# Performance work log

Hardware: AMD Instinct MI355X
Metric: run time of the kernel (lower is better)

Reference implementation:

```python
import jax, jax.numpy as jnp
import numpy as np

RENDER_STEP = 0.005
N_FREQS = 6

def pos_enc(x):
    # x: [N,3] -> [N, 3 + 2*N_FREQS*3]
    freqs = (2.0 ** jnp.arange(N_FREQS, dtype=x.dtype)) * jnp.pi
    xb = x[:, None, :] * freqs[:, None]            # [N,F,3]
    enc = jnp.concatenate([jnp.sin(xb), jnp.cos(xb)], axis=-1).reshape(x.shape[0], -1)
    return jnp.concatenate([x, enc], axis=-1)

def geom_fwd(points, Wg0, bg0, Wg1, bg1, Wg2, bg2):
    h = jax.nn.relu(pos_enc(points) @ Wg0 + bg0)
    h = jax.nn.relu(h @ Wg1 + bg1)
    return h @ Wg2 + bg2                           # [N,16]; ch0 = sdf, full vec = features


def setup_inputs() -> dict:
    key = jax.random.key(0)
    ks = jax.random.split(key, 12)
    n_rays, n_samples = 16384, 524288
    sc = lambda fan_in: 1.0 / np.sqrt(fan_in)
    inp = {
        'rays_o': jax.random.normal(ks[0], (n_rays, 3), jnp.float32) * 0.5,
        'rays_d': jax.random.normal(ks[1], (n_rays, 3), jnp.float32),
        'ray_indices': jnp.sort(jax.random.randint(ks[2], (n_samples,), 0, n_rays, jnp.int32)),
        't_starts': jax.random.uniform(ks[3], (n_samples, 1), jnp.float32),
        'random_points': jax.random.normal(ks[4], (1024, 3), jnp.float32),
        's_var': jnp.ones((1,), jnp.float32),
        'Wg0': jax.random.normal(ks[5], (39, 256), jnp.float32) * sc(39),
        'bg0': jnp.zeros((256,), jnp.float32),
        'Wg1': jax.random.normal(ks[6], (256, 256), jnp.float32) * sc(256),
        'bg1': jnp.zeros((256,), jnp.float32),
        'Wg2': jax.random.normal(ks[7], (256, 16), jnp.float32) * sc(256),
        'bg2': jnp.zeros((16,), jnp.float32),
        'Wc0': jax.random.normal(ks[8], (25, 256), jnp.float32) * sc(25),
        'bc0': jnp.zeros((256,), jnp.float32),
        'Wc1': jax.random.normal(ks[9], (256, 3), jnp.float32) * sc(256),
        'bc1': jnp.zeros((3,), jnp.float32),
    }
    return inp


def reference(rays_o, rays_d, ray_indices, t_starts, random_points, s_var,
              Wg0, bg0, Wg1, bg1, Wg2, bg2, Wc0, bc0, Wc1, bc1):
    n_rays = rays_o.shape[0]
    rays_d = rays_d / (jnp.linalg.norm(rays_d, axis=-1, keepdims=True) + 1e-10)

    midpoints = t_starts + RENDER_STEP * 0.5       # [N,1]
    t_intervals = RENDER_STEP
    t_origins = rays_o[ray_indices]                # gather [N,3]
    t_dirs = rays_d[ray_indices]
    points = t_origins + t_dirs * midpoints        # [N,3]

    # SDF network forward + analytic gradient wrt points (one fwd + one bwd)
    out, vjp_fn = jax.vjp(lambda p: geom_fwd(p, Wg0, bg0, Wg1, bg1, Wg2, bg2), points)
    sdf = out[:, 0]                                # [N]
    feats = out                                    # [N,16]
    cot = jnp.zeros_like(out).at[:, 0].set(1.0)
    grad = vjp_fn(cot)[0]                          # dSDF/dpoints [N,3]
    normal = grad / (jnp.linalg.norm(grad, axis=-1, keepdims=True) + 1e-10)

    # color network: dirs + feats + points + normal -> rgb
    cin = jnp.concatenate([t_dirs, feats, points, normal], axis=-1)   # [N,25]
    rgbs = jax.nn.sigmoid(jax.nn.relu(cin @ Wc0 + bc0) @ Wc1 + bc1)   # [N,3]

    # get_alpha (cos_anneal_ratio = 1.0)
    inv_s = jnp.clip(jnp.exp(s_var[0]), 1e-6, 1e6)
    dSDF_dt = jnp.sum(grad * t_dirs, axis=-1, keepdims=True)
    dSDF_dt = -jax.nn.relu(-dSDF_dt)
    cdf = jax.nn.sigmoid(inv_s * sdf[:, None])
    rho = jnp.maximum(inv_s * (cdf - 1.0) * dSDF_dt, 0.0)
    alpha = 1.0 - jnp.exp(-rho * t_intervals)      # [N,1]

    # render_weight_from_alpha: per-ray exclusive cumprod of (1-alpha), log-space
    a = jnp.clip(alpha[:, 0], 0.0, 1.0 - 1e-7)
    loga = jnp.log1p(-a)
    E = jnp.cumsum(loga) - loga                    # exclusive cumsum
    starts = jnp.clip(jnp.searchsorted(ray_indices, jnp.arange(n_rays, dtype=ray_indices.dtype)),
                      0, a.shape[0] - 1)           # first sample idx per ray
    trans = jnp.exp(E - E[starts][ray_indices])    # per-ray transmittance
    weights = (a * trans)[:, None]                 # [N,1]

    seg = lambda v: jax.ops.segment_sum(weights * v, ray_indices, num_segments=n_rays)
    opacity = jax.ops.segment_sum(weights, ray_indices, num_segments=n_rays)  # [R,1]
    depth = seg(midpoints)
    pixels_color = seg(rgbs)
    pixels_normal = seg(normal)
    pixels_normal = pixels_normal / (jnp.linalg.norm(pixels_normal, axis=-1, keepdims=True) + 1e-10)

    random_sdfs = geom_fwd(random_points, Wg0, bg0, Wg1, bg1, Wg2, bg2)[:, :1]
    return (pixels_color, pixels_normal, opacity, depth, weights, sdf, random_sdfs)
```

## Files before the change

kernel.cpp:

```cpp
#include <hip/hip_runtime.h>
#include <math.h>


#define TILE 32
#define NTHREADS 512
#define LDP 264
#define LDE 72
#define LDCIN 40
#define PI_F 3.14159265358979323846f

typedef _Float16 half8 __attribute__((ext_vector_type(8)));
typedef float f32x4 __attribute__((ext_vector_type(4)));
typedef float f32x16 __attribute__((ext_vector_type(16)));

struct alignas(16) SMemK2 {
    _Float16 a0h[TILE * LDP];
    _Float16 a0l[TILE * LDP];
    _Float16 a1h[TILE * LDP];
    _Float16 a1l[TILE * LDP];
    _Float16 ench[TILE * LDE];
    _Float16 encl[TILE * LDE];
    float feats[TILE * 16];
    float pts [TILE * 4];
    float dirs[TILE * 4];
    float nrm [TILE * 4];
};

__device__ __forceinline__ void splitst(float v, _Float16* ph, _Float16* pl) {
    _Float16 h = (_Float16)v;
    *ph = h;
    *pl = (_Float16)(v - (float)h);
}

__device__ __forceinline__ f32x16 zero16() {
    f32x16 z;
#pragma unroll
    for (int i = 0; i < 16; ++i) z[i] = 0.f;
    return z;
}

template<int KITERS, bool BIAS, bool RELU, bool AMASK, bool CMASK>
__device__ __forceinline__ void gemm32(
    const _Float16* Ah, const _Float16* Al, const int lda,
    const _Float16* __restrict__ Bp, const float* __restrict__ bias,
    _Float16* Ch, _Float16* Cl, const int ldc,
    const int lane, const int nt)
{
    f32x16 acc0 = zero16(), acc1 = zero16();
    const int row  = lane & 31;
    const int koff = (lane >> 5) * 8;
    const _Float16* ahb = Ah + row * lda + koff;
    const _Float16* alb = Al + row * lda + koff;
    const _Float16* bbase = Bp + ((size_t)nt * KITERS * 64 + lane) * 16;

    half8 bh[2], bl[2], ax[2], ay[2];
    bh[0] = *(const half8*)bbase;
    bl[0] = *(const half8*)(bbase + 8);
    ax[0] = *(const half8*)ahb;
    if (!AMASK) ay[0] = *(const half8*)alb;

#pragma unroll
    for (int kit = 0; kit < KITERS; ++kit) {
        const int cur = kit & 1, nxt = cur ^ 1;
        if (kit + 1 < KITERS) {
            const _Float16* bp = bbase + (size_t)(kit + 1) * 1024;
            bh[nxt] = *(const half8*)bp;
            bl[nxt] = *(const half8*)(bp + 8);
            ax[nxt] = *(const half8*)(ahb + (kit + 1) * 16);
            if (!AMASK) ay[nxt] = *(const half8*)(alb + (kit + 1) * 16);
        }
        f32x16& acc = (kit & 1) ? acc1 : acc0;
        if (AMASK) {
            half8 m;
#pragma unroll
            for (int j = 0; j < 8; ++j) {
                _Float16 t = ax[cur][j] * (_Float16)16384.f;
                m[j] = (t < (_Float16)1.f) ? t : (_Float16)1.f;
            }
            __builtin_amdgcn_s_setprio(1);
            acc = __builtin_amdgcn_mfma_f32_32x32x16_f16(m, bh[cur], acc, 0, 0, 0);
            acc = __builtin_amdgcn_mfma_f32_32x32x16_f16(m, bl[cur], acc, 0, 0, 0);
            __builtin_amdgcn_s_setprio(0);
        } else {
            __builtin_amdgcn_s_setprio(1);
            acc = __builtin_amdgcn_mfma_f32_32x32x16_f16(ay[cur], bh[cur], acc, 0, 0, 0);
            acc = __builtin_amdgcn_mfma_f32_32x32x16_f16(ax[cur], bl[cur], acc, 0, 0, 0);
            acc = __builtin_amdgcn_mfma_f32_32x32x16_f16(ax[cur], bh[cur], acc, 0, 0, 0);
            __builtin_amdgcn_s_setprio(0);
        }
    }
    const int col = lane & 31;
    const int rb  = (lane >> 5) * 4;
    const int jc  = nt * 32 + col;
    const float bs = BIAS ? bias[jc] : 0.f;
#pragma unroll
    for (int r = 0; r < 16; ++r) {
        const int srow = (r & 3) + 8 * (r >> 2) + rb;
        float v = acc0[r] + acc1[r] + bs;
        if (RELU) v = (v > 0.f) ? fmaxf(v, 1e-4f) : 0.f;
        if (CMASK) { if (!((float)Ch[srow * ldc + jc] > 0.f)) v = 0.f; }
        _Float16 h = (_Float16)v;
        Ch[srow * ldc + jc] = h;
        Cl[srow * ldc + jc] = (_Float16)(v - (float)h);
    }
}

template<int KITERS, int NTPW>
__device__ __forceinline__ void gemm16(
    const _Float16* Ah, const _Float16* Al, const int lda,
    const _Float16* __restrict__ Bp,
    _Float16* Ch, _Float16* Cl, const int ldc,
    const int lane, const int mt, const int ntbase)
{
    f32x4 acc[NTPW];
#pragma unroll
    for (int t = 0; t < NTPW; ++t) acc[t] = (f32x4){0.f, 0.f, 0.f, 0.f};
    const int m  = mt * 16 + (lane & 15);
    const int q8 = (lane >> 4) * 8;
    const _Float16* ahb = Ah + m * lda + q8;
    const _Float16* alb = Al + m * lda + q8;
    const _Float16* bbase = Bp + ((size_t)ntbase * KITERS * 64 + lane) * 16;

    half8 ax[2], ay[2], bh[2][NTPW], bl[2][NTPW];
    ax[0] = *(const half8*)ahb;
    ay[0] = *(const half8*)alb;
#pragma unroll
    for (int t = 0; t < NTPW; ++t) {
        const _Float16* bt = bbase + (size_t)t * KITERS * 1024;
        bh[0][t] = *(const half8*)bt;
        bl[0][t] = *(const half8*)(bt + 8);
    }
#pragma unroll
    for (int kit = 0; kit < KITERS; ++kit) {
        const int cur = kit & 1, nxt = cur ^ 1;
        if (kit + 1 < KITERS) {
            ax[nxt] = *(const half8*)(ahb + (kit + 1) * 32);
            ay[nxt] = *(const half8*)(alb + (kit + 1) * 32);
            const _Float16* bp = bbase + (size_t)(kit + 1) * 1024;
#pragma unroll
            for (int t = 0; t < NTPW; ++t) {
                const _Float16* bt = bp + (size_t)t * KITERS * 1024;
                bh[nxt][t] = *(const half8*)bt;
                bl[nxt][t] = *(const half8*)(bt + 8);
            }
        }
        __builtin_amdgcn_s_setprio(1);
#pragma unroll
        for (int t = 0; t < NTPW; ++t) {
            acc[t] = __builtin_amdgcn_mfma_f32_16x16x32_f16(ay[cur], bh[cur][t], acc[t], 0, 0, 0);
            acc[t] = __builtin_amdgcn_mfma_f32_16x16x32_f16(ax[cur], bl[cur][t], acc[t], 0, 0, 0);
            acc[t] = __builtin_amdgcn_mfma_f32_16x16x32_f16(ax[cur], bh[cur][t], acc[t], 0, 0, 0);
        }
        __builtin_amdgcn_s_setprio(0);
    }
    const int col = lane & 15, q = lane >> 4;
#pragma unroll
    for (int t = 0; t < NTPW; ++t) {
        const int j = (ntbase + t) * 16 + col;
#pragma unroll
        for (int r = 0; r < 4; ++r) {
            const int s = mt * 16 + q * 4 + r;
            float v = acc[t][r];
            _Float16 h = (_Float16)v;
            Ch[s * ldc + j] = h;
            Cl[s * ldc + j] = (_Float16)(v - (float)h);
        }
    }
}

__global__ __launch_bounds__(256) void k0_pack(
    const float* __restrict__ Wg0, const float* __restrict__ Wg1,
    const float* __restrict__ Wg2, const float* __restrict__ Wc0,
    const float* __restrict__ Wc1,
    _Float16* __restrict__ Wg0p, _Float16* __restrict__ Wg1p,
    _Float16* __restrict__ Wg1Tp, _Float16* __restrict__ Wg0Tp,
    _Float16* __restrict__ Wc0p, _Float16* __restrict__ Wg2p,
    _Float16* __restrict__ Wc1p)
{
    int gid = blockIdx.x * 256 + threadIdx.x;
    if (gid >= 180224) return;
    int idx, kiters, mode;
    _Float16* dst;
    if      (gid <  16384) { idx = gid;          kiters = 4;  dst = Wg0p;  mode = 0; }
    else if (gid <  81920) { idx = gid -  16384; kiters = 16; dst = Wg1p;  mode = 1; }
    else if (gid < 147456) { idx = gid -  81920; kiters = 16; dst = Wg1Tp; mode = 2; }
    else if (gid < 163840) { idx = gid - 147456; kiters = 8;  dst = Wg0Tp; mode = 3; }
    else if (gid < 172032) { idx = gid - 163840; kiters = 2;  dst = Wc0p;  mode = 4; }
    else if (gid < 176128) { idx = gid - 172032; kiters = 8;  dst = Wg2p;  mode = 5; }
    else                   { idx = gid - 176128; kiters = 8;  dst = Wc1p;  mode = 6; }
    const bool p32 = (mode == 0 || mode == 1 || mode == 2 || mode == 4);
    int j = idx & 7, lane = (idx >> 3) & 63, rest = idx >> 9;
    int kit = rest % kiters, nt = rest / kiters;
    int k, n;
    if (p32) { k = kit * 16 + ((lane >> 5) << 3) + j; n = (nt << 5) + (lane & 31); }
    else     { k = kit * 32 + ((lane >> 4) << 3) + j; n = (nt << 4) + (lane & 15); }
    float val = 0.f;
    switch (mode) {
        case 0: val = (k < 39) ? Wg0[k * 256 + n] : 0.f; break;
        case 1: val = Wg1[k * 256 + n]; break;
        case 2: val = Wg1[n * 256 + k] * Wg2[k * 16]; break;
        case 3: val = (n < 39) ? Wg0[n * 256 + k] : 0.f; break;
        case 4: val = (k < 25) ? Wc0[k * 256 + n] : 0.f; break;
        case 5: val = Wg2[k * 16 + n]; break;
        case 6: val = (n < 3) ? Wc1[k * 3 + n] : 0.f; break;
    }
    _Float16 h = (_Float16)val;
    _Float16 l = (_Float16)(val - (float)h);
    int off = ((nt * kiters + kit) * 64 + lane) * 16 + j;
    dst[off] = h;
    dst[off + 8] = l;
}

__global__ __launch_bounds__(512, 4) void k2_mlp(
    const float* __restrict__ rays_o, const float* __restrict__ rays_d,
    const int*   __restrict__ ray_idx, const float* __restrict__ t_starts,
    const float* __restrict__ s_var,
    const float* __restrict__ bg0, const float* __restrict__ bg1,
    const float* __restrict__ bg2,
    const float* __restrict__ bc0, const float* __restrict__ bc1,
    const _Float16* __restrict__ Wg0p, const _Float16* __restrict__ Wg1p,
    const _Float16* __restrict__ Wg1Tp, const _Float16* __restrict__ Wg0Tp,
    const _Float16* __restrict__ Wc0p, const _Float16* __restrict__ Wg2p,
    const _Float16* __restrict__ Wc1p,
    float* __restrict__ out_sdf, float* __restrict__ ws_a,
    float* __restrict__ ws_rgb, float* __restrict__ ws_nrm,
    int Nsamp)
{
    __shared__ SMemK2 sm;
    const int tid = threadIdx.x;
    const int lane = tid & 63;
    const int w = tid >> 6;
    const int n0 = blockIdx.x * TILE;

    if (tid < TILE) {
        int n = n0 + tid; if (n >= Nsamp) n = Nsamp - 1;
        int ri = ray_idx[n];
        float dx = rays_d[ri * 3 + 0], dy = rays_d[ri * 3 + 1], dz = rays_d[ri * 3 + 2];
        float inv = 1.f / (sqrtf(dx * dx + dy * dy + dz * dz) + 1e-10f);
        dx *= inv; dy *= inv; dz *= inv;
        float mid = t_starts[n] + 0.0025f;
        sm.dirs[tid * 4 + 0] = dx; sm.dirs[tid * 4 + 1] = dy; sm.dirs[tid * 4 + 2] = dz;
        float px = rays_o[ri * 3 + 0] + dx * mid;
        float py = rays_o[ri * 3 + 1] + dy * mid;
        float pz = rays_o[ri * 3 + 2] + dz * mid;
        sm.pts[tid * 4 + 0] = px; sm.pts[tid * 4 + 1] = py; sm.pts[tid * 4 + 2] = pz;
        splitst(px, &sm.ench[tid * LDE + 0], &sm.encl[tid * LDE + 0]);
        splitst(py, &sm.ench[tid * LDE + 1], &sm.encl[tid * LDE + 1]);
        splitst(pz, &sm.ench[tid * LDE + 2], &sm.encl[tid * LDE + 2]);
    }
    __syncthreads();

    for (int i = tid; i < TILE * 36; i += NTHREADS) {
        int s = i & (TILE - 1);
        int e = i >> 5;
        int f = e / 6, r = e - f * 6;
        float freq = PI_F * (float)(1 << f);
        int d = (r < 3) ? r : r - 3;
        float x = sm.pts[s * 4 + d];
        float v = (r < 3) ? sinf(freq * x) : cosf(freq * x);
        splitst(v, &sm.ench[s * LDE + 3 + e], &sm.encl[s * LDE + 3 + e]);
    }
    for (int i = tid; i < TILE * 25; i += NTHREADS) {
        int s = i / 25, c = 39 + (i - s * 25);
        sm.ench[s * LDE + c] = (_Float16)0.f;
        sm.encl[s * LDE + c] = (_Float16)0.f;
    }
    __syncthreads();

    gemm32<4, true, true, false, false>(sm.ench, sm.encl, LDE,
                                        Wg0p, bg0, sm.a0h, sm.a0l, LDP, lane, w);
    __syncthreads();

    gemm32<16, true, true, false, false>(sm.a0h, sm.a0l, LDP,
                                         Wg1p, bg1, sm.a1h, sm.a1l, LDP, lane, w);
    __syncthreads();

    if (w < 2) {
        f32x4 acc = (f32x4){0.f, 0.f, 0.f, 0.f};
        const int m = w * 16 + (lane & 15);
        const int q8 = (lane >> 4) * 8;
        const _Float16* ahb = sm.a1h + m * LDP + q8;
        const _Float16* alb = sm.a1l + m * LDP + q8;
        const _Float16* bbase = Wg2p + lane * 16;
        half8 ax[2], ay[2], bh[2], bl[2];
        ax[0] = *(const half8*)ahb;
        ay[0] = *(const half8*)alb;
        bh[0] = *(const half8*)bbase;
        bl[0] = *(const half8*)(bbase + 8);
#pragma unroll
        for (int kit = 0; kit < 8; ++kit) {
            const int cur = kit & 1, nxt = cur ^ 1;
            if (kit + 1 < 8) {
                ax[nxt] = *(const half8*)(ahb + (kit + 1) * 32);
                ay[nxt] = *(const half8*)(alb + (kit + 1) * 32);
                const _Float16* bp = bbase + (kit + 1) * 1024;
                bh[nxt] = *(const half8*)bp;
                bl[nxt] = *(const half8*)(bp + 8);
            }
            __builtin_amdgcn_s_setprio(1);
            acc = __builtin_amdgcn_mfma_f32_16x16x32_f16(ay[cur], bh[cur], acc, 0, 0, 0);
            acc = __builtin_amdgcn_mfma_f32_16x16x32_f16(ax[cur], bl[cur], acc, 0, 0, 0);
            acc = __builtin_amdgcn_mfma_f32_16x16x32_f16(ax[cur], bh[cur], acc, 0, 0, 0);
            __builtin_amdgcn_s_setprio(0);
        }
        int col = lane & 15, q = lane >> 4;
        float bs = bg2[col];
#pragma unroll
        for (int r = 0; r < 4; ++r) {
            int s = w * 16 + q * 4 + r;
            float vv = acc[r] + bs;
            sm.feats[s * 16 + col] = vv;
            if (col == 0) { int n = n0 + s; if (n < Nsamp) out_sdf[n] = vv; }
        }
    }

    gemm32<16, false, false, true, true>(sm.a1h, sm.a1l, LDP,
                                         Wg1Tp, nullptr, sm.a0h, sm.a0l, LDP, lane, w);
    __syncthreads();

    gemm16<8, 1>(sm.a0h, sm.a0l, LDP, Wg0Tp,
                 sm.a1h, sm.a1l, LDP, lane, w & 1, w >> 1);
    __syncthreads();

    if (tid < TILE) {
        int s = tid;
        float g[3];
#pragma unroll
        for (int d = 0; d < 3; ++d)
            g[d] = (float)sm.a1h[s * LDP + d] + (float)sm.a1l[s * LDP + d];
#pragma unroll
        for (int f = 0; f < 6; ++f) {
            float freq = PI_F * (float)(1 << f);
#pragma unroll
            for (int d = 0; d < 3; ++d) {
                int cs = 3 + f * 6 + d, cc = cs + 3;
                float gs = (float)sm.a1h[s * LDP + cs] + (float)sm.a1l[s * LDP + cs];
                float gc = (float)sm.a1h[s * LDP + cc] + (float)sm.a1l[s * LDP + cc];
                float sv = (float)sm.ench[s * LDE + cs] + (float)sm.encl[s * LDE + cs];
                float cv = (float)sm.ench[s * LDE + cc] + (float)sm.encl[s * LDE + cc];
                g[d] += freq * (gs * cv - gc * sv);
            }
        }
        float gl = sqrtf(g[0] * g[0] + g[1] * g[1] + g[2] * g[2]);
        float invl = 1.f / (gl + 1e-10f);
        float nx = g[0] * invl, ny = g[1] * invl, nz = g[2] * invl;
        sm.nrm[s * 4 + 0] = nx; sm.nrm[s * 4 + 1] = ny; sm.nrm[s * 4 + 2] = nz;
        float dx = sm.dirs[s * 4 + 0], dy = sm.dirs[s * 4 + 1], dz = sm.dirs[s * 4 + 2];
        float dsdt = fminf(g[0] * dx + g[1] * dy + g[2] * dz, 0.f);
        float sdf = sm.feats[s * 16 + 0];
        float inv_s = __expf(s_var[0]);
        inv_s = fminf(fmaxf(inv_s, 1e-6f), 1e6f);
        float cdf = 1.f / (1.f + __expf(-inv_s * sdf));
        float rho = fmaxf(inv_s * (cdf - 1.f) * dsdt, 0.f);
        float alpha = 1.f - __expf(-rho * 0.005f);
        float a = fminf(fmaxf(alpha, 0.f), 1.f - 1e-7f);
        int n = n0 + s;
        if (n < Nsamp) {
            ws_a[n] = a;
            ws_nrm[n * 3 + 0] = nx; ws_nrm[n * 3 + 1] = ny; ws_nrm[n * 3 + 2] = nz;
        }
    }
    __syncthreads();

    _Float16* cinh = sm.a0h;
    _Float16* cinl = sm.a0l;
    for (int i = tid; i < TILE * 32; i += NTHREADS) {
        int s = i >> 5, c = i & 31;
        float v = 0.f;
        if      (c < 3)  v = sm.dirs[s * 4 + c];
        else if (c < 19) v = sm.feats[s * 16 + (c - 3)];
        else if (c < 22) v = sm.pts[s * 4 + (c - 19)];
        else if (c < 25) v = sm.nrm[s * 4 + (c - 22)];
        splitst(v, &cinh[s * LDCIN + c], &cinl[s * LDCIN + c]);
    }
    __syncthreads();

    gemm32<2, true, true, false, false>(cinh, cinl, LDCIN,
                                        Wc0p, bc0, sm.a1h, sm.a1l, LDP, lane, w);
    __syncthreads();

    if (w < 2) {
        f32x4 acc = (f32x4){0.f, 0.f, 0.f, 0.f};
        const int m = w * 16 + (lane & 15);
        const int q8 = (lane >> 4) * 8;
        const _Float16* ahb = sm.a1h + m * LDP + q8;
        const _Float16* alb = sm.a1l + m * LDP + q8;
        const _Float16* bbase = Wc1p + lane * 16;
        half8 ax[2], ay[2], bh[2], bl[2];
        ax[0] = *(const half8*)ahb;
        ay[0] = *(const half8*)alb;
        bh[0] = *(const half8*)bbase;
        bl[0] = *(const half8*)(bbase + 8);
#pragma unroll
        for (int kit = 0; kit < 8; ++kit) {
            const int cur = kit & 1, nxt = cur ^ 1;
            if (kit + 1 < 8) {
                ax[nxt] = *(const half8*)(ahb + (kit + 1) * 32);
                ay[nxt] = *(const half8*)(alb + (kit + 1) * 32);
                const _Float16* bp = bbase + (kit + 1) * 1024;
                bh[nxt] = *(const half8*)bp;
                bl[nxt] = *(const half8*)(bp + 8);
            }
            __builtin_amdgcn_s_setprio(1);
            acc = __builtin_amdgcn_mfma_f32_16x16x32_f16(ay[cur], bh[cur], acc, 0, 0, 0);
            acc = __builtin_amdgcn_mfma_f32_16x16x32_f16(ax[cur], bl[cur], acc, 0, 0, 0);
            acc = __builtin_amdgcn_mfma_f32_16x16x32_f16(ax[cur], bh[cur], acc, 0, 0, 0);
            __builtin_amdgcn_s_setprio(0);
        }
        int col = lane & 15, q = lane >> 4;
        if (col < 3) {
#pragma unroll
            for (int r = 0; r < 4; ++r) {
                int s = w * 16 + q * 4 + r;
                float rgb = 1.f / (1.f + __expf(-(acc[r] + bc1[col])));
                int n = n0 + s;
                if (n < Nsamp) ws_rgb[n * 3 + col] = rgb;
            }
        }
    }
}

__global__ void k3_composite(
    const int* __restrict__ ray_idx, const float* __restrict__ t_starts,
    const float* __restrict__ ws_a, const float* __restrict__ ws_rgb,
    const float* __restrict__ ws_nrm,
    float* __restrict__ out_pc, float* __restrict__ out_pn,
    float* __restrict__ out_op, float* __restrict__ out_dp,
    float* __restrict__ out_w, int n_rays, int Nsamp)
{
    int r = blockIdx.x * blockDim.x + threadIdx.x;
    if (r >= n_rays) return;
    int lo = 0, hi = Nsamp;
    while (lo < hi) { int m = (lo + hi) >> 1; if (ray_idx[m] < r) lo = m + 1; else hi = m; }
    int start = lo;
    hi = Nsamp;
    while (lo < hi) { int m = (lo + hi) >> 1; if (ray_idx[m] < r + 1) lo = m + 1; else hi = m; }
    int end = lo;

    float T = 1.f, aco = 0.f, acd = 0.f;
    float c0 = 0.f, c1 = 0.f, c2 = 0.f, nx = 0.f, ny = 0.f, nz = 0.f;
    for (int n = start; n < end; ++n) {
        float a = ws_a[n];
        float wgt = a * T;
        T *= (1.f - a);
        out_w[n] = wgt;
        float mid = t_starts[n] + 0.0025f;
        aco += wgt; acd += wgt * mid;
        c0 += wgt * ws_rgb[n * 3 + 0];
        c1 += wgt * ws_rgb[n * 3 + 1];
        c2 += wgt * ws_rgb[n * 3 + 2];
        nx += wgt * ws_nrm[n * 3 + 0];
        ny += wgt * ws_nrm[n * 3 + 1];
        nz += wgt * ws_nrm[n * 3 + 2];
    }
    out_op[r] = aco;
    out_dp[r] = acd;
    out_pc[r * 3 + 0] = c0; out_pc[r * 3 + 1] = c1; out_pc[r * 3 + 2] = c2;
    float nl = sqrtf(nx * nx + ny * ny + nz * nz);
    float inv = 1.f / (nl + 1e-10f);
    out_pn[r * 3 + 0] = nx * inv; out_pn[r * 3 + 1] = ny * inv; out_pn[r * 3 + 2] = nz * inv;
}

__global__ __launch_bounds__(256) void k4_random(
    const float* __restrict__ pts,
    const float* __restrict__ Wg0, const float* __restrict__ bg0,
    const float* __restrict__ Wg1, const float* __restrict__ bg1,
    const float* __restrict__ Wg2, const float* __restrict__ bg2,
    float* __restrict__ out_rs, int n_rand)
{
    __shared__ float enc[40];
    __shared__ float h[256];
    __shared__ float red[256];
    int b = blockIdx.x;
    if (b >= n_rand) return;
    int tid = threadIdx.x;
    if (tid < 39) {
        int c = tid;
        float v;
        if (c < 3) v = pts[b * 3 + c];
        else {
            int e = c - 3, f = e / 6, r = e - f * 6;
            float freq = PI_F * (float)(1 << f);
            int d = (r < 3) ? r : r - 3;
            float x = pts[b * 3 + d];
            v = (r < 3) ? sinf(freq * x) : cosf(freq * x);
        }
        enc[c] = v;
    }
    __syncthreads();
    {
        float z = bg0[tid];
        for (int m = 0; m < 39; ++m) z += enc[m] * Wg0[m * 256 + tid];
        h[tid] = fmaxf(z, 0.f);
    }
    __syncthreads();
    {
        float z = bg1[tid];
        for (int k = 0; k < 256; ++k) z += h[k] * Wg1[k * 256 + tid];
        float h1 = fmaxf(z, 0.f);
        red[tid] = h1 * Wg2[tid * 16];
    }
    __syncthreads();
    for (int off = 128; off > 0; off >>= 1) {
        if (tid < off) red[tid] += red[tid + off];
        __syncthreads();
    }
    if (tid == 0) out_rs[b] = red[0] + bg2[0];
}

extern "C" void kernel_launch(void* const* d_in, const int* in_sizes, int n_in,
                              void* d_out, int out_size, void* d_ws, size_t ws_size,
                              hipStream_t stream)
{
    const float* rays_o   = (const float*)d_in[0];
    const float* rays_d   = (const float*)d_in[1];
    const int*   ray_idx  = (const int*)  d_in[2];
    const float* t_starts = (const float*)d_in[3];
    const float* rpts     = (const float*)d_in[4];
    const float* s_var    = (const float*)d_in[5];
    const float* Wg0 = (const float*)d_in[6];  const float* bg0 = (const float*)d_in[7];
    const float* Wg1 = (const float*)d_in[8];  const float* bg1 = (const float*)d_in[9];
    const float* Wg2 = (const float*)d_in[10]; const float* bg2 = (const float*)d_in[11];
    const float* Wc0 = (const float*)d_in[12]; const float* bc0 = (const float*)d_in[13];
    const float* Wc1 = (const float*)d_in[14]; const float* bc1 = (const float*)d_in[15];

    const int n_rays = in_sizes[0] / 3;
    const int Ns     = in_sizes[2];
    const int n_rand = in_sizes[4] / 3;

    float* out  = (float*)d_out;
    float* o_pc = out;
    float* o_pn = out + (size_t)3 * n_rays;
    float* o_op = out + (size_t)6 * n_rays;
    float* o_dp = out + (size_t)7 * n_rays;
    float* o_w  = out + (size_t)8 * n_rays;
    float* o_sdf = o_w + Ns;
    float* o_rs  = o_sdf + Ns;

    _Float16* hptr  = (_Float16*)d_ws;
    _Float16* Wg0p  = hptr;
    _Float16* Wg1p  = Wg0p  + 32768;
    _Float16* Wg1Tp = Wg1p  + 131072;
    _Float16* Wg0Tp = Wg1Tp + 131072;
    _Float16* Wc0p  = Wg0Tp + 32768;
    _Float16* Wg2p  = Wc0p  + 16384;
    _Float16* Wc1p  = Wg2p  + 8192;
    float* fbase  = (float*)(hptr + 360448);
    float* ws_a   = fbase;
    float* ws_rgb = ws_a + Ns;
    float* ws_nrm = ws_rgb + (size_t)3 * Ns;

    hipLaunchKernelGGL(k0_pack, dim3(704), dim3(256), 0, stream,
                       Wg0, Wg1, Wg2, Wc0, Wc1,
                       Wg0p, Wg1p, Wg1Tp, Wg0Tp, Wc0p, Wg2p, Wc1p);
    hipLaunchKernelGGL(k2_mlp, dim3((Ns + TILE - 1) / TILE), dim3(NTHREADS), 0, stream,
                       rays_o, rays_d, ray_idx, t_starts, s_var,
                       bg0, bg1, bg2, bc0, bc1,
                       Wg0p, Wg1p, Wg1Tp, Wg0Tp, Wc0p, Wg2p, Wc1p,
                       o_sdf, ws_a, ws_rgb, ws_nrm, Ns);
    hipLaunchKernelGGL(k4_random, dim3(n_rand), dim3(256), 0, stream,
                       rpts, Wg0, bg0, Wg1, bg1, Wg2, bg2, o_rs, n_rand);
    hipLaunchKernelGGL(k3_composite, dim3((n_rays + 255) / 256), dim3(256), 0, stream,
                       ray_idx, t_starts, ws_a, ws_rgb, ws_nrm,
                       o_pc, o_pn, o_op, o_dp, o_w, n_rays, Ns);
}
```

Measured before the change: 774.9 us.

## Trim padded K, drop masked low-part MFMA, sin/cos recurrence, deeper B prefetch

Reduces the first-layer K padding from 64 to 48 (three K iterations instead of four) and repacks the weights to match. The positional encoding now computes one sin/cos per coordinate and derives the higher frequencies with double-angle recurrences instead of calling sinf/cosf for every frequency. The masked backward GEMM drops the multiply against the low half of the weights, and the B-operand prefetch goes from two stages to three. These cut MFMA count, transcendental calls and load latency, but the recurrence accumulates rounding error and dropping the low-half product lowers the precision of the masked GEMM.

```diff
diff --git a/kernel.cpp b/kernel.cpp
--- a/kernel.cpp
+++ b/kernel.cpp
@@ -39,7 +39,7 @@
     return z;
 }
 
-template<int KITERS, bool BIAS, bool RELU, bool AMASK, bool CMASK>
+template<int KITERS, bool BIAS, bool RELU, bool AMASK, bool CMASK, bool WLO>
 __device__ __forceinline__ void gemm32(
     const _Float16* Ah, const _Float16* Al, const int lda,
     const _Float16* __restrict__ Bp, const float* __restrict__ bias,
@@ -53,39 +53,47 @@
     const _Float16* alb = Al + row * lda + koff;
     const _Float16* bbase = Bp + ((size_t)nt * KITERS * 64 + lane) * 16;
 
-    half8 bh[2], bl[2], ax[2], ay[2];
-    bh[0] = *(const half8*)bbase;
-    bl[0] = *(const half8*)(bbase + 8);
+    half8 ax[2], ay[2];
+    half8 bh[3], bl[3];
     ax[0] = *(const half8*)ahb;
     if (!AMASK) ay[0] = *(const half8*)alb;
+    bh[0] = *(const half8*)bbase;
+    if (!AMASK) bl[0] = *(const half8*)(bbase + 8);
+    if (KITERS > 1) {
+        bh[1] = *(const half8*)(bbase + 1024);
+        if (!AMASK) bl[1] = *(const half8*)(bbase + 1024 + 8);
+    }
 
 #pragma unroll
     for (int kit = 0; kit < KITERS; ++kit) {
-        const int cur = kit & 1, nxt = cur ^ 1;
+        const int ac = kit & 1, an = ac ^ 1;
+        const int bc = kit % 3;
         if (kit + 1 < KITERS) {
-            const _Float16* bp = bbase + (size_t)(kit + 1) * 1024;
-            bh[nxt] = *(const half8*)bp;
-            bl[nxt] = *(const half8*)(bp + 8);
-            ax[nxt] = *(const half8*)(ahb + (kit + 1) * 16);
-            if (!AMASK) ay[nxt] = *(const half8*)(alb + (kit + 1) * 16);
-        }
-        f32x16& acc = (kit & 1) ? acc1 : acc0;
+            ax[an] = *(const half8*)(ahb + (kit + 1) * 16);
+            if (!AMASK) ay[an] = *(const half8*)(alb + (kit + 1) * 16);
+        }
+        if (kit + 2 < KITERS) {
+            const int bn = (kit + 2) % 3;
+            const _Float16* bp = bbase + (size_t)(kit + 2) * 1024;
+            bh[bn] = *(const half8*)bp;
+            if (!AMASK) bl[bn] = *(const half8*)(bp + 8);
+        }
+        f32x16& acc = ac ? acc1 : acc0;
         if (AMASK) {
             half8 m;
 #pragma unroll
             for (int j = 0; j < 8; ++j) {
-                _Float16 t = ax[cur][j] * (_Float16)16384.f;
+                _Float16 t = ax[ac][j] * (_Float16)16384.f;
                 m[j] = (t < (_Float16)1.f) ? t : (_Float16)1.f;
             }
             __builtin_amdgcn_s_setprio(1);
-            acc = __builtin_amdgcn_mfma_f32_32x32x16_f16(m, bh[cur], acc, 0, 0, 0);
-            acc = __builtin_amdgcn_mfma_f32_32x32x16_f16(m, bl[cur], acc, 0, 0, 0);
+            acc = __builtin_amdgcn_mfma_f32_32x32x16_f16(m, bh[bc], acc, 0, 0, 0);
             __builtin_amdgcn_s_setprio(0);
         } else {
             __builtin_amdgcn_s_setprio(1);
-            acc = __builtin_amdgcn_mfma_f32_32x32x16_f16(ay[cur], bh[cur], acc, 0, 0, 0);
-            acc = __builtin_amdgcn_mfma_f32_32x32x16_f16(ax[cur], bl[cur], acc, 0, 0, 0);
-            acc = __builtin_amdgcn_mfma_f32_32x32x16_f16(ax[cur], bh[cur], acc, 0, 0, 0);
+            acc = __builtin_amdgcn_mfma_f32_32x32x16_f16(ay[ac], bh[bc], acc, 0, 0, 0);
+            acc = __builtin_amdgcn_mfma_f32_32x32x16_f16(ax[ac], bl[bc], acc, 0, 0, 0);
+            acc = __builtin_amdgcn_mfma_f32_32x32x16_f16(ax[ac], bh[bc], acc, 0, 0, 0);
             __builtin_amdgcn_s_setprio(0);
         }
     }
@@ -101,7 +109,7 @@
         if (CMASK) { if (!((float)Ch[srow * ldc + jc] > 0.f)) v = 0.f; }
         _Float16 h = (_Float16)v;
         Ch[srow * ldc + jc] = h;
-        Cl[srow * ldc + jc] = (_Float16)(v - (float)h);
+        if (WLO) Cl[srow * ldc + jc] = (_Float16)(v - (float)h);
     }
 }
 
@@ -121,7 +129,7 @@
     const _Float16* alb = Al + m * lda + q8;
     const _Float16* bbase = Bp + ((size_t)ntbase * KITERS * 64 + lane) * 16;
 
-    half8 ax[2], ay[2], bh[2][NTPW], bl[2][NTPW];
+    half8 ax[2], ay[2], bh[3][NTPW], bl[3][NTPW];
     ax[0] = *(const half8*)ahb;
     ay[0] = *(const half8*)alb;
 #pragma unroll
@@ -130,26 +138,38 @@
         bh[0][t] = *(const half8*)bt;
         bl[0][t] = *(const half8*)(bt + 8);
     }
+    if (KITERS > 1) {
+#pragma unroll
+        for (int t = 0; t < NTPW; ++t) {
+            const _Float16* bt = bbase + 1024 + (size_t)t * KITERS * 1024;
+            bh[1][t] = *(const half8*)bt;
+            bl[1][t] = *(const half8*)(bt + 8);
+        }
+    }
 #pragma unroll
     for (int kit = 0; kit < KITERS; ++kit) {
-        const int cur = kit & 1, nxt = cur ^ 1;
+        const int ac = kit & 1, an = ac ^ 1;
+        const int bc = kit % 3;
         if (kit + 1 < KITERS) {
-            ax[nxt] = *(const half8*)(ahb + (kit + 1) * 32);
-            ay[nxt] = *(const half8*)(alb + (kit + 1) * 32);
-            const _Float16* bp = bbase + (size_t)(kit + 1) * 1024;
+            ax[an] = *(const half8*)(ahb + (kit + 1) * 32);
+            ay[an] = *(const half8*)(alb + (kit + 1) * 32);
+        }
+        if (kit + 2 < KITERS) {
+            const int bn = (kit + 2) % 3;
+            const _Float16* bp = bbase + (size_t)(kit + 2) * 1024;
 #pragma unroll
             for (int t = 0; t < NTPW; ++t) {
                 const _Float16* bt = bp + (size_t)t * KITERS * 1024;
-                bh[nxt][t] = *(const half8*)bt;
-                bl[nxt][t] = *(const half8*)(bt + 8);
+                bh[bn][t] = *(const half8*)bt;
+                bl[bn][t] = *(const half8*)(bt + 8);
             }
         }
         __builtin_amdgcn_s_setprio(1);
 #pragma unroll
         for (int t = 0; t < NTPW; ++t) {
-            acc[t] = __builtin_amdgcn_mfma_f32_16x16x32_f16(ay[cur], bh[cur][t], acc[t], 0, 0, 0);
-            acc[t] = __builtin_amdgcn_mfma_f32_16x16x32_f16(ax[cur], bl[cur][t], acc[t], 0, 0, 0);
-            acc[t] = __builtin_amdgcn_mfma_f32_16x16x32_f16(ax[cur], bh[cur][t], acc[t], 0, 0, 0);
+            acc[t] = __builtin_amdgcn_mfma_f32_16x16x32_f16(ay[ac], bh[bc][t], acc[t], 0, 0, 0);
+            acc[t] = __builtin_amdgcn_mfma_f32_16x16x32_f16(ax[ac], bl[bc][t], acc[t], 0, 0, 0);
+            acc[t] = __builtin_amdgcn_mfma_f32_16x16x32_f16(ax[ac], bh[bc][t], acc[t], 0, 0, 0);
         }
         __builtin_amdgcn_s_setprio(0);
     }
@@ -178,16 +198,16 @@
     _Float16* __restrict__ Wc1p)
 {
     int gid = blockIdx.x * 256 + threadIdx.x;
-    if (gid >= 180224) return;
+    if (gid >= 176128) return;
     int idx, kiters, mode;
     _Float16* dst;
-    if      (gid <  16384) { idx = gid;          kiters = 4;  dst = Wg0p;  mode = 0; }
-    else if (gid <  81920) { idx = gid -  16384; kiters = 16; dst = Wg1p;  mode = 1; }
-    else if (gid < 147456) { idx = gid -  81920; kiters = 16; dst = Wg1Tp; mode = 2; }
-    else if (gid < 163840) { idx = gid - 147456; kiters = 8;  dst = Wg0Tp; mode = 3; }
-    else if (gid < 172032) { idx = gid - 163840; kiters = 2;  dst = Wc0p;  mode = 4; }
-    else if (gid < 176128) { idx = gid - 172032; kiters = 8;  dst = Wg2p;  mode = 5; }
-    else                   { idx = gid - 176128; kiters = 8;  dst = Wc1p;  mode = 6; }
+    if      (gid <  12288) { idx = gid;          kiters = 3;  dst = Wg0p;  mode = 0; }
+    else if (gid <  77824) { idx = gid -  12288; kiters = 16; dst = Wg1p;  mode = 1; }
+    else if (gid < 143360) { idx = gid -  77824; kiters = 16; dst = Wg1Tp; mode = 2; }
+    else if (gid < 159744) { idx = gid - 143360; kiters = 8;  dst = Wg0Tp; mode = 3; }
+    else if (gid < 167936) { idx = gid - 159744; kiters = 2;  dst = Wc0p;  mode = 4; }
+    else if (gid < 172032) { idx = gid - 167936; kiters = 8;  dst = Wg2p;  mode = 5; }
+    else                   { idx = gid - 172032; kiters = 8;  dst = Wc1p;  mode = 6; }
     const bool p32 = (mode == 0 || mode == 1 || mode == 2 || mode == 4);
     int j = idx & 7, lane = (idx >> 3) & 63, rest = idx >> 9;
     int kit = rest % kiters, nt = rest / kiters;
@@ -250,29 +270,34 @@
     }
     __syncthreads();
 
-    for (int i = tid; i < TILE * 36; i += NTHREADS) {
-        int s = i & (TILE - 1);
-        int e = i >> 5;
-        int f = e / 6, r = e - f * 6;
-        float freq = PI_F * (float)(1 << f);
-        int d = (r < 3) ? r : r - 3;
+    for (int i = tid; i < TILE * 3; i += NTHREADS) {
+        int s = i & 31;
+        int d = i >> 5;
         float x = sm.pts[s * 4 + d];
-        float v = (r < 3) ? sinf(freq * x) : cosf(freq * x);
-        splitst(v, &sm.ench[s * LDE + 3 + e], &sm.encl[s * LDE + 3 + e]);
-    }
-    for (int i = tid; i < TILE * 25; i += NTHREADS) {
-        int s = i / 25, c = 39 + (i - s * 25);
+        float a = PI_F * x;
+        float sv = sinf(a), cv = cosf(a);
+#pragma unroll
+        for (int f = 0; f < 6; ++f) {
+            splitst(sv, &sm.ench[s * LDE + 3 + f * 6 + d],     &sm.encl[s * LDE + 3 + f * 6 + d]);
+            splitst(cv, &sm.ench[s * LDE + 3 + f * 6 + 3 + d], &sm.encl[s * LDE + 3 + f * 6 + 3 + d]);
+            float s2 = 2.f * sv * cv;
+            float c2 = 1.f - 2.f * sv * sv;
+            sv = s2; cv = c2;
+        }
+    }
+    for (int i = tid; i < TILE * 9; i += NTHREADS) {
+        int s = i / 9, c = 39 + (i - s * 9);
         sm.ench[s * LDE + c] = (_Float16)0.f;
         sm.encl[s * LDE + c] = (_Float16)0.f;
     }
     __syncthreads();
 
-    gemm32<4, true, true, false, false>(sm.ench, sm.encl, LDE,
-                                        Wg0p, bg0, sm.a0h, sm.a0l, LDP, lane, w);
-    __syncthreads();
-
-    gemm32<16, true, true, false, false>(sm.a0h, sm.a0l, LDP,
-                                         Wg1p, bg1, sm.a1h, sm.a1l, LDP, lane, w);
+    gemm32<3, true, true, false, false, true>(sm.ench, sm.encl, LDE,
+                                              Wg0p, bg0, sm.a0h, sm.a0l, LDP, lane, w);
+    __syncthreads();
+
+    gemm32<16, true, true, false, false, true>(sm.a0h, sm.a0l, LDP,
+                                               Wg1p, bg1, sm.a1h, sm.a1l, LDP, lane, w);
     __syncthreads();
 
     if (w < 2) {
@@ -314,8 +339,8 @@
         }
     }
 
-    gemm32<16, false, false, true, true>(sm.a1h, sm.a1l, LDP,
-                                         Wg1Tp, nullptr, sm.a0h, sm.a0l, LDP, lane, w);
+    gemm32<16, false, false, true, true, true>(sm.a1h, sm.a1l, LDP,
+                                               Wg1Tp, nullptr, sm.a0h, sm.a0l, LDP, lane, w);
     __syncthreads();
 
     gemm16<8, 1>(sm.a0h, sm.a0l, LDP, Wg0Tp,
@@ -375,8 +400,8 @@
     }
     __syncthreads();
 
-    gemm32<2, true, true, false, false>(cinh, cinl, LDCIN,
-                                        Wc0p, bc0, sm.a1h, sm.a1l, LDP, lane, w);
+    gemm32<2, true, true, false, false, true>(cinh, cinl, LDCIN,
+                                              Wc0p, bc0, sm.a1h, sm.a1l, LDP, lane, w);
     __syncthreads();
 
     if (w < 2) {
@@ -539,18 +564,18 @@
 
     _Float16* hptr  = (_Float16*)d_ws;
     _Float16* Wg0p  = hptr;
-    _Float16* Wg1p  = Wg0p  + 32768;
+    _Float16* Wg1p  = Wg0p  + 24576;
     _Float16* Wg1Tp = Wg1p  + 131072;
     _Float16* Wg0Tp = Wg1Tp + 131072;
     _Float16* Wc0p  = Wg0Tp + 32768;
     _Float16* Wg2p  = Wc0p  + 16384;
     _Float16* Wc1p  = Wg2p  + 8192;
-    float* fbase  = (float*)(hptr + 360448);
+    float* fbase  = (float*)(hptr + 352256);
     float* ws_a   = fbase;
     float* ws_rgb = ws_a + Ns;
     float* ws_nrm = ws_rgb + (size_t)3 * Ns;
 
-    hipLaunchKernelGGL(k0_pack, dim3(704), dim3(256), 0, stream,
+    hipLaunchKernelGGL(k0_pack, dim3(688), dim3(256), 0, stream,
                        Wg0, Wg1, Wg2, Wc0, Wc1,
                        Wg0p, Wg1p, Wg1Tp, Wg0Tp, Wc0p, Wg2p, Wc1p);
     hipLaunchKernelGGL(k2_mlp, dim3((Ns + TILE - 1) / TILE), dim3(NTHREADS), 0, stream,
```

After: 712.2 us. 1.09x faster.
